# Kernel optimization log

Hardware: AMD Instinct MI355X
Metric: run time of the kernel (lower is better)

## Reference

```python
import jax, jax.numpy as jnp
import numpy as np

B, R, U, D = 16, 2048, 2048, 1024
EPS_ATT = 1e-8
EPS_LN = 1e-6


def setup_inputs() -> dict:
    key = jax.random.key(0)
    ks = jax.random.split(key, 6)
    s = 1.0 / np.sqrt(D)
    return {
        "Q": jax.random.normal(ks[0], (B, R, D), dtype=jnp.float32),
        "K": jax.random.normal(ks[1], (B, U, D), dtype=jnp.float32),
        "V": jax.random.normal(ks[2], (B, U, D), dtype=jnp.float32),
        "W1": jax.random.normal(ks[3], (D, D), dtype=jnp.float32) * s,
        "b1": jnp.zeros((D,), dtype=jnp.float32),
        "W2": jax.random.normal(ks[4], (D, D), dtype=jnp.float32) * s,
        "b2": jnp.zeros((D,), dtype=jnp.float32),
        "gamma": jnp.ones((D,), dtype=jnp.float32),
        "beta": jnp.zeros((D,), dtype=jnp.float32),
    }


def reference(Q, K, V, W1, b1, W2, b2, gamma, beta):
    d_model = Q.shape[-1]
    # Faithful to source: sqrt(d_model + epsilon)
    scale = jnp.sqrt(jnp.asarray(d_model, jnp.float32) + EPS_ATT)
    scores = jnp.einsum('brd,bud->bru', Q, K) / scale  # [B,R,U]
    att = jax.nn.softmax(scores, axis=-1)
    V_att = jnp.einsum('bru,bud->brd', att, V)  # [B,R,D]

    def layer_norm(x):
        mu = jnp.mean(x, axis=-1, keepdims=True)
        var = jnp.mean(jnp.square(x - mu), axis=-1, keepdims=True)
        return gamma * (x - mu) / jnp.sqrt(var + EPS_LN) + beta

    X = layer_norm(Q + V_att)
    ffn = jnp.maximum(X @ W1 + b1, 0.0) @ W2 + b2
    return layer_norm(ffn + X)
```

## Files before the change

### kernel.cpp

```cpp
#include <hip/hip_runtime.h>
#include <math.h>
#include <stdint.h>

#define BATCH 16
#define RDIM 2048
#define UDIM 2048
#define DDIM 1024

typedef __attribute__((ext_vector_type(8))) short short8;
typedef __attribute__((ext_vector_type(4))) float f32x4;
typedef __attribute__((ext_vector_type(8))) unsigned short ushort8;
typedef __attribute__((ext_vector_type(4))) unsigned short ushort4v;
typedef __attribute__((ext_vector_type(4))) float float4v;

__device__ __forceinline__ float bf2f(unsigned short u) {
  unsigned int x = ((unsigned int)u) << 16;
  return __builtin_bit_cast(float, x);
}
__device__ __forceinline__ unsigned short f2bf(float f) {
  unsigned int x = __builtin_bit_cast(unsigned int, f);
  unsigned int r = (x + 0x7fffu + ((x >> 16) & 1u)) >> 16;
  return (unsigned short)r;
}

__device__ __forceinline__ void gload_lds16(const void* g, void* l) {
  __builtin_amdgcn_global_load_lds(
      (const __attribute__((address_space(1))) void*)(uintptr_t)g,
      (__attribute__((address_space(3))) void*)(uint32_t)(uintptr_t)l,
      16, 0, 0);
}

#define FENCE() __builtin_amdgcn_sched_barrier(0)
#define BAR() __builtin_amdgcn_s_barrier()
#define LGKM0() asm volatile("s_waitcnt lgkmcnt(0)" ::: "memory")
#define LGKM8() asm volatile("s_waitcnt lgkmcnt(8)" ::: "memory")
#define VMCNT6() asm volatile("s_waitcnt vmcnt(6)" ::: "memory")
#define VMCNT0() asm volatile("s_waitcnt vmcnt(0)" ::: "memory")


__global__ __launch_bounds__(256) void k_conv_bf16(const float* __restrict__ in,
                                                   unsigned short* __restrict__ out,
                                                   float scale) {
  const long i = ((long)blockIdx.x * 256 + threadIdx.x) * 8;
  float4v a = *(const float4v*)(in + i);
  float4v b = *(const float4v*)(in + i + 4);
  ushort8 o;
#pragma unroll
  for (int j = 0; j < 4; ++j) o[j] = f2bf(a[j] * scale);
#pragma unroll
  for (int j = 0; j < 4; ++j) o[4 + j] = f2bf(b[j] * scale);
  *(ushort8*)(out + i) = o;
}

__global__ void k_transpose_bf16(const float* __restrict__ in,
                                 unsigned short* __restrict__ out,
                                 int rows, int cols, long sIn, long sOut) {
  __shared__ unsigned short tile[64][65];
  const long bz = blockIdx.z;
  in += bz * sIn;
  out += bz * sOut;
  const int r0 = blockIdx.x * 64;
  const int c0 = blockIdx.y * 64;
  const int tx = threadIdx.x;
  const int ty = threadIdx.y;
#pragma unroll
  for (int i = 0; i < 16; ++i) {
    const int r = ty + i * 4;
    tile[r][tx] = f2bf(in[(long)(r0 + r) * cols + c0 + tx]);
  }
  __syncthreads();
#pragma unroll
  for (int i = 0; i < 16; ++i) {
    const int r = ty + i * 4;
    out[(long)(c0 + r) * rows + r0 + tx] = tile[tx][r];
  }
}


template <int EPI>
__global__ __launch_bounds__(512, 1) void gemm_bt(
    const unsigned short* __restrict__ A, const unsigned short* __restrict__ B,
    void* __restrict__ Cout, int N, int K, long sA, long sB, long sC,
    const float* __restrict__ bias, const unsigned short* __restrict__ res) {
  __shared__ __align__(128) unsigned short lds[2][2][2][256 * 32];

  int lin = blockIdx.x + gridDim.x * (blockIdx.y + gridDim.y * blockIdx.z);
  lin = (lin & 7) * ((gridDim.x * gridDim.y * gridDim.z) >> 3) + (lin >> 3);
  const int by = lin % gridDim.y;
  int rest = lin / gridDim.y;
  const int bx = rest % gridDim.x;
  const int bz = rest / gridDim.x;

  const unsigned short* Ab = A + (long)bz * sA;
  const unsigned short* Bb = B + (long)bz * sB;

  const int tid = threadIdx.x;
  const int w = tid >> 6;
  const int lane = tid & 63;
  const int wm = w >> 2;
  const int wn = w & 3;
  const long rowBase = (long)bx * 256;
  const long colBase = (long)by * 256;

  const int s = tid >> 2;
  const int kslot = (tid & 3) ^ ((tid >> 3) & 3);
  const int lRowA = s + (s & 64);
  const int lRowB = ((s & 96) << 1) + (s & 31);
  const unsigned short* gA0 = Ab + (long)(rowBase + lRowA) * K + kslot * 8;
  const unsigned short* gB0 = Bb + (long)(colBase + lRowB) * K + kslot * 8;
  char* ldsB = (char*)&lds[0][0][0][0];
  const int wOff = w * 1024;

  auto STAGE_A = [&](int buf, int h, int kt) {
    const unsigned short* g = gA0 + (long)(h * 64) * K + kt * 64;
    char* d = ldsB + ((buf * 4 + 0) << 14) + h * 8192 + wOff;
    gload_lds16(g, d);
    gload_lds16(g + 32, d + 16384);
  };
  auto STAGE_B = [&](int buf, int h, int kt) {
    const unsigned short* g = gB0 + (long)(h * 32) * K + kt * 64;
    char* d = ldsB + ((buf * 4 + 2) << 14) + h * 8192 + wOff;
    gload_lds16(g, d);
    gload_lds16(g + 32, d + 16384);
  };

  const int laneM = lane & 15;
  const int laneQ = lane >> 4;
  const int swz = (laneQ ^ ((laneM >> 1) & 3)) << 4;
  const int rdA = (wm * 64 + laneM) * 64 + swz;
  const int rdB = (wn * 32 + laneM) * 64 + swz;

  f32x4 acc[8][4] = {};
  const int NT = K >> 6;
  const int NI = NT >> 1;

  short8 A0[4][2], A1[4][2], B0[2][2], B1[2][2];

  auto RD_A = [&](short8 (&dst)[4][2], int buf, int h) {
#pragma unroll
    for (int mm = 0; mm < 4; ++mm)
#pragma unroll
      for (int kk = 0; kk < 2; ++kk)
        dst[mm][kk] = *(const short8*)(ldsB + ((buf * 4 + kk) << 14) +
                                       h * 8192 + rdA + mm * 1024);
  };
  auto RD_B = [&](short8 (&dst)[2][2], int buf, int h) {
#pragma unroll
    for (int nn = 0; nn < 2; ++nn)
#pragma unroll
      for (int kk = 0; kk < 2; ++kk)
        dst[nn][kk] = *(const short8*)(ldsB + ((buf * 4 + 2 + kk) << 14) +
                                       h * 8192 + rdB + nn * 1024);
  };

#define MFMAQ(AF, BF, MB, NB)                                                  \
  __builtin_amdgcn_s_setprio(1);                                               \
  _Pragma("unroll") for (int mm = 0; mm < 4; ++mm)                             \
  _Pragma("unroll") for (int nn = 0; nn < 2; ++nn)                             \
  _Pragma("unroll") for (int kk = 0; kk < 2; ++kk)                             \
      acc[MB + mm][NB + nn] = __builtin_amdgcn_mfma_f32_16x16x32_bf16(         \
          AF[mm][kk], BF[nn][kk], acc[MB + mm][NB + nn], 0, 0, 0);             \
  __builtin_amdgcn_s_setprio(0);

  STAGE_A(0, 0, 0); STAGE_B(0, 0, 0); STAGE_B(0, 1, 0); STAGE_A(0, 1, 0);
  STAGE_A(1, 0, 1); STAGE_B(1, 0, 1); STAGE_B(1, 1, 1);
  VMCNT6();
  BAR();
  FENCE();

  for (int i = 0; i < NI; ++i) {
    const int t1 = 2 * i + 1;
    const int t2 = (2 * i + 2 <= NT - 1) ? 2 * i + 2 : NT - 1;
    const int t3 = (2 * i + 3 <= NT - 1) ? 2 * i + 3 : NT - 1;

    RD_A(A0, 0, 0); RD_B(B0, 0, 0);
    STAGE_A(1, 1, t1);
    LGKM8(); BAR(); LGKM0(); FENCE();
    MFMAQ(A0, B0, 0, 0);
    BAR();

    RD_B(B1, 0, 1);
    STAGE_A(0, 0, t2);
    BAR(); LGKM0(); FENCE();
    MFMAQ(A0, B1, 0, 2);
    BAR();

    RD_A(A1, 0, 1);
    STAGE_B(0, 0, t2);
    BAR(); LGKM0(); FENCE();
    MFMAQ(A1, B1, 4, 2);
    BAR();

    STAGE_B(0, 1, t2);
    VMCNT6(); BAR(); FENCE();
    MFMAQ(A1, B0, 4, 0);
    BAR();

    RD_A(A0, 1, 0); RD_B(B0, 1, 0);
    STAGE_A(0, 1, t2);
    LGKM8(); BAR(); LGKM0(); FENCE();
    MFMAQ(A0, B0, 0, 0);
    BAR();

    RD_B(B1, 1, 1);
    STAGE_A(1, 0, t3);
    BAR(); LGKM0(); FENCE();
    MFMAQ(A0, B1, 0, 2);
    BAR();

    RD_A(A1, 1, 1);
    STAGE_B(1, 0, t3);
    BAR(); LGKM0(); FENCE();
    MFMAQ(A1, B1, 4, 2);
    BAR();

    STAGE_B(1, 1, t3);
    VMCNT6(); BAR(); FENCE();
    MFMAQ(A1, B0, 4, 0);
    BAR();
  }
  VMCNT0();
#undef MFMAQ

  const long r0 = rowBase + wm * 128;
  const long c0 = colBase + wn * 64;
  const int cr = (lane >> 4) << 2;
  const int cc = lane & 15;

  if constexpr (EPI == 0) {
    unsigned short* C = (unsigned short*)Cout + (long)bz * sC;
#pragma unroll
    for (int i = 0; i < 8; ++i)
#pragma unroll
      for (int j = 0; j < 4; ++j)
#pragma unroll
        for (int jj = 0; jj < 4; ++jj)
          C[(r0 + i * 16 + cr + jj) * N + (c0 + j * 16 + cc)] = f2bf(acc[i][j][jj]);
  } else if constexpr (EPI == 1) {
    unsigned short* C = (unsigned short*)Cout;
#pragma unroll
    for (int i = 0; i < 8; ++i)
#pragma unroll
      for (int j = 0; j < 4; ++j)
#pragma unroll
        for (int jj = 0; jj < 4; ++jj) {
          const long col = c0 + j * 16 + cc;
          float v = acc[i][j][jj] + bias[col];
          v = fmaxf(v, 0.f);
          C[(r0 + i * 16 + cr + jj) * N + col] = f2bf(v);
        }
  } else {
    float* C = (float*)Cout;
#pragma unroll
    for (int i = 0; i < 8; ++i)
#pragma unroll
      for (int j = 0; j < 4; ++j)
#pragma unroll
        for (int jj = 0; jj < 4; ++jj) {
          const long row = r0 + i * 16 + cr + jj;
          const long col = c0 + j * 16 + cc;
          C[row * N + col] = acc[i][j][jj] + bias[col] + bf2f(res[row * N + col]);
        }
  }
}


__global__ __launch_bounds__(256) void k_softmax(unsigned short* __restrict__ S) {
  __shared__ float red[8];
  const long base = (long)blockIdx.x * UDIM;
  const int t = threadIdx.x;
  ushort8 raw = *(const ushort8*)(S + base + t * 8);
  float v[8];
  float mx = -3.0e38f;
#pragma unroll
  for (int j = 0; j < 8; ++j) {
    v[j] = bf2f(raw[j]);
    mx = fmaxf(mx, v[j]);
  }
#pragma unroll
  for (int m = 32; m >= 1; m >>= 1) mx = fmaxf(mx, __shfl_xor(mx, m));
  const int wv = t >> 6;
  if ((t & 63) == 0) red[wv] = mx;
  __syncthreads();
  mx = fmaxf(fmaxf(red[0], red[1]), fmaxf(red[2], red[3]));
  float s = 0.f;
#pragma unroll
  for (int j = 0; j < 8; ++j) {
    v[j] = __expf(v[j] - mx);
    s += v[j];
  }
#pragma unroll
  for (int m = 32; m >= 1; m >>= 1) s += __shfl_xor(s, m);
  if ((t & 63) == 0) red[4 + wv] = s;
  __syncthreads();
  s = red[4] + red[5] + red[6] + red[7];
  const float rs = 1.f / s;
  ushort8 o;
#pragma unroll
  for (int j = 0; j < 8; ++j) o[j] = f2bf(v[j] * rs);
  *(ushort8*)(S + base + t * 8) = o;
}


__global__ __launch_bounds__(256) void k_addln_bf16(
    const float* __restrict__ Q, const unsigned short* __restrict__ Va,
    unsigned short* __restrict__ X, const float* __restrict__ gamma,
    const float* __restrict__ beta) {
  __shared__ float red[8];
  const long base = (long)blockIdx.x * DDIM;
  const int t = threadIdx.x;
  float4v q = *(const float4v*)(Q + base + t * 4);
  ushort4v a = *(const ushort4v*)(Va + base + t * 4);
  float x[4];
  float s = 0.f, ss = 0.f;
#pragma unroll
  for (int j = 0; j < 4; ++j) {
    x[j] = q[j] + bf2f(a[j]);
    s += x[j];
    ss += x[j] * x[j];
  }
#pragma unroll
  for (int m = 32; m >= 1; m >>= 1) {
    s += __shfl_xor(s, m);
    ss += __shfl_xor(ss, m);
  }
  const int wv = t >> 6;
  if ((t & 63) == 0) {
    red[wv] = s;
    red[4 + wv] = ss;
  }
  __syncthreads();
  s = red[0] + red[1] + red[2] + red[3];
  ss = red[4] + red[5] + red[6] + red[7];
  const float mu = s * (1.f / DDIM);
  const float var = ss * (1.f / DDIM) - mu * mu;
  const float rstd = rsqrtf(var + 1e-6f);
  ushort4v o;
#pragma unroll
  for (int j = 0; j < 4; ++j) {
    const int c = t * 4 + j;
    o[j] = f2bf(gamma[c] * ((x[j] - mu) * rstd) + beta[c]);
  }
  *(ushort4v*)(X + base + t * 4) = o;
}


__global__ __launch_bounds__(256) void k_ln_inplace(float* __restrict__ Y,
                                                    const float* __restrict__ gamma,
                                                    const float* __restrict__ beta) {
  __shared__ float red[8];
  const long base = (long)blockIdx.x * DDIM;
  const int t = threadIdx.x;
  float4v y = *(const float4v*)(Y + base + t * 4);
  float s = 0.f, ss = 0.f;
#pragma unroll
  for (int j = 0; j < 4; ++j) {
    s += y[j];
    ss += y[j] * y[j];
  }
#pragma unroll
  for (int m = 32; m >= 1; m >>= 1) {
    s += __shfl_xor(s, m);
    ss += __shfl_xor(ss, m);
  }
  const int wv = t >> 6;
  if ((t & 63) == 0) {
    red[wv] = s;
    red[4 + wv] = ss;
  }
  __syncthreads();
  s = red[0] + red[1] + red[2] + red[3];
  ss = red[4] + red[5] + red[6] + red[7];
  const float mu = s * (1.f / DDIM);
  const float var = ss * (1.f / DDIM) - mu * mu;
  const float rstd = rsqrtf(var + 1e-6f);
  float4v o;
#pragma unroll
  for (int j = 0; j < 4; ++j) {
    const int c = t * 4 + j;
    o[j] = gamma[c] * ((y[j] - mu) * rstd) + beta[c];
  }
  *(float4v*)(Y + base + t * 4) = o;
}


extern "C" void kernel_launch(void* const* d_in, const int* in_sizes, int n_in,
                              void* d_out, int out_size, void* d_ws, size_t ws_size,
                              hipStream_t stream) {
  const float* Q = (const float*)d_in[0];
  const float* Kin = (const float*)d_in[1];
  const float* V = (const float*)d_in[2];
  const float* W1 = (const float*)d_in[3];
  const float* b1 = (const float*)d_in[4];
  const float* W2 = (const float*)d_in[5];
  const float* b2 = (const float*)d_in[6];
  const float* gamma = (const float*)d_in[7];
  const float* beta = (const float*)d_in[8];
  float* out = (float*)d_out;

  const long nQ = (long)BATCH * RDIM * DDIM;
  const long nK = (long)BATCH * UDIM * DDIM;
  const long nS = (long)BATCH * RDIM * UDIM;

  char* w = (char*)d_ws;
  unsigned short* Qb = (unsigned short*)w;  w += nQ * 2;
  unsigned short* Kb = (unsigned short*)w;  w += nK * 2;
  unsigned short* Vt = (unsigned short*)w;  w += nK * 2;
  unsigned short* S  = (unsigned short*)w;  w += nS * 2;
  unsigned short* X  = (unsigned short*)w;  w += nQ * 2;
  unsigned short* W1t = (unsigned short*)w; w += (long)DDIM * DDIM * 2;
  unsigned short* W2t = (unsigned short*)w; w += (long)DDIM * DDIM * 2;
  unsigned short* Va = Qb;
  unsigned short* H  = S;

  const float scale = 1.0f / sqrtf(1024.0f + 1e-8f);

  k_conv_bf16<<<nQ / 2048, 256, 0, stream>>>(Q, Qb, scale);
  k_conv_bf16<<<nK / 2048, 256, 0, stream>>>(Kin, Kb, 1.0f);
  k_transpose_bf16<<<dim3(UDIM / 64, DDIM / 64, BATCH), dim3(64, 4), 0, stream>>>(
      V, Vt, UDIM, DDIM, (long)UDIM * DDIM, (long)UDIM * DDIM);
  k_transpose_bf16<<<dim3(DDIM / 64, DDIM / 64, 1), dim3(64, 4), 0, stream>>>(
      W1, W1t, DDIM, DDIM, 0, 0);
  k_transpose_bf16<<<dim3(DDIM / 64, DDIM / 64, 1), dim3(64, 4), 0, stream>>>(
      W2, W2t, DDIM, DDIM, 0, 0);

  gemm_bt<0><<<dim3(RDIM / 256, UDIM / 256, BATCH), 512, 0, stream>>>(
      Qb, Kb, S, UDIM, DDIM, (long)RDIM * DDIM, (long)UDIM * DDIM, (long)RDIM * UDIM,
      nullptr, nullptr);
  k_softmax<<<BATCH * RDIM, 256, 0, stream>>>(S);
  gemm_bt<0><<<dim3(RDIM / 256, DDIM / 256, BATCH), 512, 0, stream>>>(
      S, Vt, Va, DDIM, UDIM, (long)RDIM * UDIM, (long)DDIM * UDIM, (long)RDIM * DDIM,
      nullptr, nullptr);
  k_addln_bf16<<<BATCH * RDIM, 256, 0, stream>>>(Q, Va, X, gamma, beta);
  gemm_bt<1><<<dim3(BATCH * RDIM / 256, DDIM / 256, 1), 512, 0, stream>>>(
      X, W1t, H, DDIM, DDIM, 0, 0, 0, b1, nullptr);
  gemm_bt<2><<<dim3(BATCH * RDIM / 256, DDIM / 256, 1), 512, 0, stream>>>(
      H, W2t, out, DDIM, DDIM, 0, 0, 0, b2, X);
  k_ln_inplace<<<BATCH * RDIM, 256, 0, stream>>>(out, gamma, beta);
}
```

Before: 660.0 us.

## Fuse softmax exp and row sums into QK GEMM, LN stats into FFN2 epilogue

The QK^T GEMM epilogue now writes exp(scores) without subtracting the row max and emits per-tile row-sum partials. Normalization is deferred to the add+LayerNorm kernel, which scales the un-normalized PV result by the reciprocal sum. The separate softmax pass over the full score matrix is removed. The second FFN GEMM now writes bf16 output and per-row sum and sum-of-squares partials, so the final LayerNorm becomes a single light pass, and the Q and K conversions are merged into one launch. Skipping max subtraction risks overflow for larger score ranges, and the bf16 intermediate before the final LayerNorm adds rounding error.

```diff
diff --git a/kernel.cpp b/kernel.cpp
--- a/kernel.cpp
+++ b/kernel.cpp
@@ -38,17 +38,22 @@
 #define VMCNT0() asm volatile("s_waitcnt vmcnt(0)" ::: "memory")
 
 
-__global__ __launch_bounds__(256) void k_conv_bf16(const float* __restrict__ in,
-                                                   unsigned short* __restrict__ out,
-                                                   float scale) {
+__global__ __launch_bounds__(256) void k_conv2(const float* __restrict__ Q,
+                                               const float* __restrict__ Kin,
+                                               unsigned short* __restrict__ Qb,
+                                               unsigned short* __restrict__ Kb,
+                                               float scale) {
+  const float* in = blockIdx.y ? Kin : Q;
+  unsigned short* out = blockIdx.y ? Kb : Qb;
+  const float s = blockIdx.y ? 1.0f : scale;
   const long i = ((long)blockIdx.x * 256 + threadIdx.x) * 8;
   float4v a = *(const float4v*)(in + i);
   float4v b = *(const float4v*)(in + i + 4);
   ushort8 o;
 #pragma unroll
-  for (int j = 0; j < 4; ++j) o[j] = f2bf(a[j] * scale);
-#pragma unroll
-  for (int j = 0; j < 4; ++j) o[4 + j] = f2bf(b[j] * scale);
+  for (int j = 0; j < 4; ++j) o[j] = f2bf(a[j] * s);
+#pragma unroll
+  for (int j = 0; j < 4; ++j) o[4 + j] = f2bf(b[j] * s);
   *(ushort8*)(out + i) = o;
 }
 
@@ -81,7 +86,8 @@
 __global__ __launch_bounds__(512, 1) void gemm_bt(
     const unsigned short* __restrict__ A, const unsigned short* __restrict__ B,
     void* __restrict__ Cout, int N, int K, long sA, long sB, long sC,
-    const float* __restrict__ bias, const unsigned short* __restrict__ res) {
+    const float* __restrict__ bias, const unsigned short* __restrict__ res,
+    float* __restrict__ part) {
   __shared__ __align__(128) unsigned short lds[2][2][2][256 * 32];
 
   int lin = blockIdx.x + gridDim.x * (blockIdx.y + gridDim.y * blockIdx.z);
@@ -220,12 +226,13 @@
     BAR();
   }
   VMCNT0();
+  BAR();
 #undef MFMAQ
 
   const long r0 = rowBase + wm * 128;
   const long c0 = colBase + wn * 64;
-  const int cr = (lane >> 4) << 2;
-  const int cc = lane & 15;
+  const int cr = laneQ << 2;
+  const int cc = laneM;
 
   if constexpr (EPI == 0) {
     unsigned short* C = (unsigned short*)Cout + (long)bz * sC;
@@ -249,8 +256,47 @@
           v = fmaxf(v, 0.f);
           C[(r0 + i * 16 + cr + jj) * N + col] = f2bf(v);
         }
+  } else if constexpr (EPI == 3) {
+    unsigned short* C = (unsigned short*)Cout + (long)bz * sC;
+    float rp[8][4];
+#pragma unroll
+    for (int i = 0; i < 8; ++i)
+#pragma unroll
+      for (int jj = 0; jj < 4; ++jj) rp[i][jj] = 0.f;
+#pragma unroll
+    for (int i = 0; i < 8; ++i)
+#pragma unroll
+      for (int j = 0; j < 4; ++j)
+#pragma unroll
+        for (int jj = 0; jj < 4; ++jj) {
+          float e = __expf(acc[i][j][jj]);
+          C[(r0 + i * 16 + cr + jj) * N + (c0 + j * 16 + cc)] = f2bf(e);
+          rp[i][jj] += e;
+        }
+    float* sm = (float*)ldsB;
+#pragma unroll
+    for (int i = 0; i < 8; ++i)
+#pragma unroll
+      for (int jj = 0; jj < 4; ++jj) {
+        float r4 = rp[i][jj];
+        r4 += __shfl_xor(r4, 8);
+        r4 += __shfl_xor(r4, 4);
+        r4 += __shfl_xor(r4, 2);
+        r4 += __shfl_xor(r4, 1);
+        if (cc == 0) sm[wn * 256 + wm * 128 + i * 16 + cr + jj] = r4;
+      }
+    BAR();
+    if (tid < 256) {
+      float ssum = sm[tid] + sm[256 + tid] + sm[512 + tid] + sm[768 + tid];
+      part[((long)bz * RDIM + rowBase + tid) * 8 + by] = ssum;
+    }
   } else {
-    float* C = (float*)Cout;
+    unsigned short* C = (unsigned short*)Cout;
+    float rp1[8][4], rp2[8][4];
+#pragma unroll
+    for (int i = 0; i < 8; ++i)
+#pragma unroll
+      for (int jj = 0; jj < 4; ++jj) { rp1[i][jj] = 0.f; rp2[i][jj] = 0.f; }
 #pragma unroll
     for (int i = 0; i < 8; ++i)
 #pragma unroll
@@ -259,63 +305,55 @@
         for (int jj = 0; jj < 4; ++jj) {
           const long row = r0 + i * 16 + cr + jj;
           const long col = c0 + j * 16 + cc;
-          C[row * N + col] = acc[i][j][jj] + bias[col] + bf2f(res[row * N + col]);
+          float v = acc[i][j][jj] + bias[col] + bf2f(res[row * N + col]);
+          C[row * N + col] = f2bf(v);
+          rp1[i][jj] += v;
+          rp2[i][jj] += v * v;
         }
-  }
-}
-
-
-__global__ __launch_bounds__(256) void k_softmax(unsigned short* __restrict__ S) {
-  __shared__ float red[8];
-  const long base = (long)blockIdx.x * UDIM;
-  const int t = threadIdx.x;
-  ushort8 raw = *(const ushort8*)(S + base + t * 8);
-  float v[8];
-  float mx = -3.0e38f;
-#pragma unroll
-  for (int j = 0; j < 8; ++j) {
-    v[j] = bf2f(raw[j]);
-    mx = fmaxf(mx, v[j]);
-  }
-#pragma unroll
-  for (int m = 32; m >= 1; m >>= 1) mx = fmaxf(mx, __shfl_xor(mx, m));
-  const int wv = t >> 6;
-  if ((t & 63) == 0) red[wv] = mx;
-  __syncthreads();
-  mx = fmaxf(fmaxf(red[0], red[1]), fmaxf(red[2], red[3]));
-  float s = 0.f;
-#pragma unroll
-  for (int j = 0; j < 8; ++j) {
-    v[j] = __expf(v[j] - mx);
-    s += v[j];
-  }
-#pragma unroll
-  for (int m = 32; m >= 1; m >>= 1) s += __shfl_xor(s, m);
-  if ((t & 63) == 0) red[4 + wv] = s;
-  __syncthreads();
-  s = red[4] + red[5] + red[6] + red[7];
-  const float rs = 1.f / s;
-  ushort8 o;
-#pragma unroll
-  for (int j = 0; j < 8; ++j) o[j] = f2bf(v[j] * rs);
-  *(ushort8*)(S + base + t * 8) = o;
+    float* sm = (float*)ldsB;
+#pragma unroll
+    for (int i = 0; i < 8; ++i)
+#pragma unroll
+      for (int jj = 0; jj < 4; ++jj) {
+        float r4 = rp1[i][jj], q4 = rp2[i][jj];
+        r4 += __shfl_xor(r4, 8); q4 += __shfl_xor(q4, 8);
+        r4 += __shfl_xor(r4, 4); q4 += __shfl_xor(q4, 4);
+        r4 += __shfl_xor(r4, 2); q4 += __shfl_xor(q4, 2);
+        r4 += __shfl_xor(r4, 1); q4 += __shfl_xor(q4, 1);
+        if (cc == 0) {
+          sm[wn * 256 + wm * 128 + i * 16 + cr + jj] = r4;
+          sm[1024 + wn * 256 + wm * 128 + i * 16 + cr + jj] = q4;
+        }
+      }
+    BAR();
+    if (tid < 256) {
+      float s1 = sm[tid] + sm[256 + tid] + sm[512 + tid] + sm[768 + tid];
+      float s2 = sm[1024 + tid] + sm[1280 + tid] + sm[1536 + tid] + sm[1792 + tid];
+      part[(rowBase + tid) * 8 + by * 2] = s1;
+      part[(rowBase + tid) * 8 + by * 2 + 1] = s2;
+    }
+  }
 }
 
 
 __global__ __launch_bounds__(256) void k_addln_bf16(
     const float* __restrict__ Q, const unsigned short* __restrict__ Va,
     unsigned short* __restrict__ X, const float* __restrict__ gamma,
-    const float* __restrict__ beta) {
+    const float* __restrict__ beta, const float* __restrict__ rsP) {
   __shared__ float red[8];
-  const long base = (long)blockIdx.x * DDIM;
+  const long row = blockIdx.x;
+  const long base = row * DDIM;
   const int t = threadIdx.x;
+  const float* p = rsP + row * 8;
+  const float rs =
+      1.0f / (((p[0] + p[1]) + (p[2] + p[3])) + ((p[4] + p[5]) + (p[6] + p[7])));
   float4v q = *(const float4v*)(Q + base + t * 4);
   ushort4v a = *(const ushort4v*)(Va + base + t * 4);
   float x[4];
   float s = 0.f, ss = 0.f;
 #pragma unroll
   for (int j = 0; j < 4; ++j) {
-    x[j] = q[j] + bf2f(a[j]);
+    x[j] = q[j] + bf2f(a[j]) * rs;
     s += x[j];
     ss += x[j] * x[j];
   }
@@ -345,42 +383,27 @@
 }
 
 
-__global__ __launch_bounds__(256) void k_ln_inplace(float* __restrict__ Y,
-                                                    const float* __restrict__ gamma,
-                                                    const float* __restrict__ beta) {
-  __shared__ float red[8];
-  const long base = (long)blockIdx.x * DDIM;
+__global__ __launch_bounds__(256) void k_ln_final(
+    const unsigned short* __restrict__ y, const float* __restrict__ lnP,
+    float* __restrict__ out, const float* __restrict__ gamma,
+    const float* __restrict__ beta) {
+  const long row = blockIdx.x;
+  const long base = row * DDIM;
   const int t = threadIdx.x;
-  float4v y = *(const float4v*)(Y + base + t * 4);
-  float s = 0.f, ss = 0.f;
-#pragma unroll
-  for (int j = 0; j < 4; ++j) {
-    s += y[j];
-    ss += y[j] * y[j];
-  }
-#pragma unroll
-  for (int m = 32; m >= 1; m >>= 1) {
-    s += __shfl_xor(s, m);
-    ss += __shfl_xor(ss, m);
-  }
-  const int wv = t >> 6;
-  if ((t & 63) == 0) {
-    red[wv] = s;
-    red[4 + wv] = ss;
-  }
-  __syncthreads();
-  s = red[0] + red[1] + red[2] + red[3];
-  ss = red[4] + red[5] + red[6] + red[7];
-  const float mu = s * (1.f / DDIM);
-  const float var = ss * (1.f / DDIM) - mu * mu;
+  const float* p = lnP + row * 8;
+  const float s1 = (p[0] + p[2]) + (p[4] + p[6]);
+  const float s2 = (p[1] + p[3]) + (p[5] + p[7]);
+  const float mu = s1 * (1.f / DDIM);
+  const float var = s2 * (1.f / DDIM) - mu * mu;
   const float rstd = rsqrtf(var + 1e-6f);
+  ushort4v v = *(const ushort4v*)(y + base + t * 4);
   float4v o;
 #pragma unroll
   for (int j = 0; j < 4; ++j) {
     const int c = t * 4 + j;
-    o[j] = gamma[c] * ((y[j] - mu) * rstd) + beta[c];
-  }
-  *(float4v*)(Y + base + t * 4) = o;
+    o[j] = gamma[c] * ((bf2f(v[j]) - mu) * rstd) + beta[c];
+  }
+  *(float4v*)(out + base + t * 4) = o;
 }
 
 
@@ -401,6 +424,7 @@
   const long nQ = (long)BATCH * RDIM * DDIM;
   const long nK = (long)BATCH * UDIM * DDIM;
   const long nS = (long)BATCH * RDIM * UDIM;
+  const long nRows = (long)BATCH * RDIM;
 
   char* w = (char*)d_ws;
   unsigned short* Qb = (unsigned short*)w;  w += nQ * 2;
@@ -410,13 +434,14 @@
   unsigned short* X  = (unsigned short*)w;  w += nQ * 2;
   unsigned short* W1t = (unsigned short*)w; w += (long)DDIM * DDIM * 2;
   unsigned short* W2t = (unsigned short*)w; w += (long)DDIM * DDIM * 2;
+  float* partP = (float*)w;                 w += nRows * 8 * 4;
   unsigned short* Va = Qb;
   unsigned short* H  = S;
+  unsigned short* Y  = Kb;
 
   const float scale = 1.0f / sqrtf(1024.0f + 1e-8f);
 
-  k_conv_bf16<<<nQ / 2048, 256, 0, stream>>>(Q, Qb, scale);
-  k_conv_bf16<<<nK / 2048, 256, 0, stream>>>(Kin, Kb, 1.0f);
+  k_conv2<<<dim3(nQ / 2048, 2), 256, 0, stream>>>(Q, Kin, Qb, Kb, scale);
   k_transpose_bf16<<<dim3(UDIM / 64, DDIM / 64, BATCH), dim3(64, 4), 0, stream>>>(
       V, Vt, UDIM, DDIM, (long)UDIM * DDIM, (long)UDIM * DDIM);
   k_transpose_bf16<<<dim3(DDIM / 64, DDIM / 64, 1), dim3(64, 4), 0, stream>>>(
@@ -424,17 +449,16 @@
   k_transpose_bf16<<<dim3(DDIM / 64, DDIM / 64, 1), dim3(64, 4), 0, stream>>>(
       W2, W2t, DDIM, DDIM, 0, 0);
 
-  gemm_bt<0><<<dim3(RDIM / 256, UDIM / 256, BATCH), 512, 0, stream>>>(
+  gemm_bt<3><<<dim3(RDIM / 256, UDIM / 256, BATCH), 512, 0, stream>>>(
       Qb, Kb, S, UDIM, DDIM, (long)RDIM * DDIM, (long)UDIM * DDIM, (long)RDIM * UDIM,
-      nullptr, nullptr);
-  k_softmax<<<BATCH * RDIM, 256, 0, stream>>>(S);
+      nullptr, nullptr, partP);
   gemm_bt<0><<<dim3(RDIM / 256, DDIM / 256, BATCH), 512, 0, stream>>>(
       S, Vt, Va, DDIM, UDIM, (long)RDIM * UDIM, (long)DDIM * UDIM, (long)RDIM * DDIM,
-      nullptr, nullptr);
-  k_addln_bf16<<<BATCH * RDIM, 256, 0, stream>>>(Q, Va, X, gamma, beta);
+      nullptr, nullptr, nullptr);
+  k_addln_bf16<<<nRows, 256, 0, stream>>>(Q, Va, X, gamma, beta, partP);
   gemm_bt<1><<<dim3(BATCH * RDIM / 256, DDIM / 256, 1), 512, 0, stream>>>(
-      X, W1t, H, DDIM, DDIM, 0, 0, 0, b1, nullptr);
-  gemm_bt<2><<<dim3(BATCH * RDIM / 256, DDIM / 256, 1), 512, 0, stream>>>(
-      H, W2t, out, DDIM, DDIM, 0, 0, 0, b2, X);
-  k_ln_inplace<<<BATCH * RDIM, 256, 0, stream>>>(out, gamma, beta);
-}
+      X, W1t, H, DDIM, DDIM, 0, 0, 0, b1, nullptr, nullptr);
+  gemm_bt<4><<<dim3(BATCH * RDIM / 256, DDIM / 256, 1), 512, 0, stream>>>(
+      H, W2t, Y, DDIM, DDIM, 0, 0, 0, b2, X, partP);
+  k_ln_final<<<nRows, 256, 0, stream>>>(Y, partP, out, gamma, beta);
+}
```

After: 631.9 us. 1.04x faster.
